# Kernel optimization log

Hardware: AMD Instinct MI355X
Metric: run time of the kernel (lower is better)

The kernel has to match this reference:

```python
import jax, jax.numpy as jnp
import numpy as np

N = 100000       # nodes
E = 3200000      # directed edges (before self-loops)
F_IN = 256       # num_node_features
HID = 8          # hidden per head (conv1)
HEADS = 8        # conv1 heads
C_OUT = 1        # conv2 out channels / heads=1


def setup_inputs() -> dict:
    key = jax.random.key(0)
    ks = jax.random.split(key, 10)
    s = 0.1
    return {
        "x": jax.random.normal(ks[0], (N, F_IN), jnp.float32),
        "edge_index": jax.random.randint(ks[1], (2, E), 0, N, dtype=jnp.int32),
        "W1": jax.random.normal(ks[2], (F_IN, HEADS * HID), jnp.float32) * s,
        "att_src1": jax.random.normal(ks[3], (HEADS, HID), jnp.float32) * s,
        "att_dst1": jax.random.normal(ks[4], (HEADS, HID), jnp.float32) * s,
        "b1": jnp.zeros((HEADS * HID,), jnp.float32),
        "W2": jax.random.normal(ks[5], (HEADS * HID, C_OUT), jnp.float32) * s,
        "att_src2": jax.random.normal(ks[6], (1, C_OUT), jnp.float32) * s,
        "att_dst2": jax.random.normal(ks[7], (1, C_OUT), jnp.float32) * s,
        "b2": jnp.zeros((C_OUT,), jnp.float32),
    }


def gat_conv(x, W, att_src, att_dst, bias, src, dst, heads, out_ch, concat):
    # PyG GATConv (eval mode): h = x @ W per head; alpha over incoming edges of dst.
    h = (x @ W).reshape(-1, heads, out_ch)                 # [N, H, C]
    a_s = jnp.einsum('nhc,hc->nh', h, att_src)             # source term
    a_d = jnp.einsum('nhc,hc->nh', h, att_dst)             # target term
    e = jax.nn.leaky_relu(a_s[src] + a_d[dst], 0.2)        # [Etot, H]
    # segment softmax over edges grouped by target node
    m = jax.ops.segment_max(e, dst, num_segments=N)
    ex = jnp.exp(e - m[dst])
    denom = jax.ops.segment_sum(ex, dst, num_segments=N)
    alpha = ex / (denom[dst] + 1e-16)                      # [Etot, H]
    out = jax.ops.segment_sum(h[src] * alpha[..., None], dst, num_segments=N)
    out = out.reshape(-1, heads * out_ch) if concat else out.mean(axis=1)
    return out + bias


def reference(x, edge_index, W1, att_src1, att_dst1, b1, W2, att_src2, att_dst2, b2):
    # add self-loops (GATConv default add_self_loops=True)
    loop = jnp.arange(N, dtype=edge_index.dtype)
    src = jnp.concatenate([edge_index[0], loop])
    dst = jnp.concatenate([edge_index[1], loop])
    # dropout layers are identity in eval mode
    h = gat_conv(x, W1, att_src1, att_dst1, b1, src, dst, HEADS, HID, True)
    h = jax.nn.elu(h)
    out = gat_conv(h, W2, att_src2, att_dst2, b2, src, dst, 1, C_OUT, False)
    return jax.nn.sigmoid(out)
```

## Files before the change

kernel.cpp:

```cpp
#include <hip/hip_runtime.h>
#include <math.h>

#define FIN 256
#define C1  64
#define NH  8
#define HID 8
#define MAXBUK 512
#define CAPLOG 14
#define SC_CHUNK 8192
#define EPT (SC_CHUNK / 512)
#define WT_STRIDE 264

typedef unsigned short ushort_t;
typedef unsigned int uint_t;
typedef __attribute__((ext_vector_type(8))) short short8;
typedef __attribute__((ext_vector_type(4))) float f32x4;

__device__ __forceinline__ ushort_t f2bf(float f) {
    uint_t u = __float_as_uint(f);
    u += 0x7fffu + ((u >> 16) & 1u);
    return (ushort_t)(u >> 16);
}
__device__ __forceinline__ uint_t packbf2(float lo, float hi) {
    return (uint_t)f2bf(lo) | ((uint_t)f2bf(hi) << 16);
}
__device__ __forceinline__ float bf_lo(uint_t w) { return __uint_as_float(w << 16); }
__device__ __forceinline__ float bf_hi(uint_t w) { return __uint_as_float(w & 0xffff0000u); }

__global__ void k_zero_i(int* __restrict__ p, int n) {
    int i = blockIdx.x * blockDim.x + threadIdx.x;
    if (i < n) p[i] = 0;
}

__global__ __launch_bounds__(512) void k_bscatter(const int* __restrict__ ei, int E, int N,
                                                  int NBUK, int* __restrict__ bkt_cnt,
                                                  uint_t* __restrict__ ebuf) {
    __shared__ int hist[MAXBUK];
    __shared__ int loff[MAXBUK];
    __shared__ int delta[MAXBUK];
    __shared__ int ssum[MAXBUK];
    __shared__ uint_t vals[SC_CHUNK];
    __shared__ ushort_t buks[SC_CHUNK];

    const int t = threadIdx.x;
    hist[t] = 0;
    __syncthreads();

    const int Etot = E + N;
    const int base0 = blockIdx.x * SC_CHUNK;
    const int lim = min(base0 + SC_CHUNK, Etot);
    const int cnt = lim - base0;

    uint_t myval[EPT];
    int myb[EPT];
#pragma unroll
    for (int i = 0; i < EPT; ++i) {
        int e = base0 + t + i * 512;
        if (e < lim) {
            int s, d;
            if (e < E) { s = ei[e]; d = ei[E + e]; } else { s = e - E; d = s; }
            myval[i] = ((uint_t)s << 8) | (uint_t)(d & 255);
            myb[i] = d >> 8;
            atomicAdd(&hist[myb[i]], 1);
        } else myb[i] = -1;
    }
    __syncthreads();

    int v = hist[t];
    ssum[t] = v;
    __syncthreads();
    for (int o = 1; o < 512; o <<= 1) {
        int add = (t >= o) ? ssum[t - o] : 0;
        __syncthreads();
        ssum[t] += add;
        __syncthreads();
    }
    loff[t] = ssum[t] - v;
    __syncthreads();

    if (t < NBUK) {
        int c = hist[t];
        if (c) delta[t] = (t << CAPLOG) + atomicAdd(&bkt_cnt[t], c) - loff[t];
    }
    __syncthreads();

#pragma unroll
    for (int i = 0; i < EPT; ++i) {
        if (myb[i] >= 0) {
            int pos = atomicAdd(&loff[myb[i]], 1);
            vals[pos] = myval[i];
            buks[pos] = (ushort_t)myb[i];
        }
    }
    __syncthreads();

    for (int i = t; i < cnt; i += 512)
        ebuf[delta[buks[i]] + i] = vals[i];
}

__global__ __launch_bounds__(512) void k_bucket_csr(const uint_t* __restrict__ ebuf,
                                                    const int* __restrict__ bkt_cnt, int N,
                                                    int* __restrict__ deg, int* __restrict__ off,
                                                    int* __restrict__ csr) {
    __shared__ int degw[8 * 256];
    __shared__ int scan[256];
    __shared__ int curl[256];
    int b = blockIdx.x;
    int t = threadIdx.x;
    int wv = t >> 6;
    int beg = b << CAPLOG;
    int end = beg + bkt_cnt[b];
    for (int i = t; i < 8 * 256; i += 512) degw[i] = 0;
    __syncthreads();
    for (int j = beg + t; j < end; j += 512) {
        uint_t v = ebuf[j];
        atomicAdd(&degw[(wv << 8) + (v & 255u)], 1);
    }
    __syncthreads();
    int v = 0;
    if (t < 256) {
#pragma unroll
        for (int w = 0; w < 8; ++w) v += degw[(w << 8) + t];
        scan[t] = v;
    }
    __syncthreads();
    for (int o = 1; o < 256; o <<= 1) {
        int a = (t < 256 && t >= o) ? scan[t - o] : 0;
        __syncthreads();
        if (t < 256) scan[t] += a;
        __syncthreads();
    }
    if (t < 256) {
        int gpos = beg + scan[t] - v;
        int node = (b << 8) + t;
        if (node < N) { off[node] = gpos; deg[node] = v; }
        curl[t] = gpos;
    }
    __syncthreads();
    for (int j = beg + t; j < end; j += 512) {
        uint_t p = ebuf[j];
        int pos = atomicAdd(&curl[p & 255u], 1);
        csr[pos] = (int)(p >> 8);
    }
}

__global__ __launch_bounds__(256) void k_gemm1(
    const float* __restrict__ x, const float* __restrict__ W,
    const float* __restrict__ att_s, const float* __restrict__ att_d,
    ushort_t* __restrict__ h1b, ushort_t* __restrict__ as1b, float* __restrict__ ad1, int N)
{
    __shared__ __align__(16) ushort_t Wt[C1 * WT_STRIDE];

    const int t = threadIdx.x;
    {
        int c4 = t >> 4;
        int k0 = t & 15;
#pragma unroll
        for (int i = 0; i < 16; ++i) {
            int k = k0 + 16 * i;
            float4 v = *reinterpret_cast<const float4*>(&W[k * C1 + c4 * 4]);
            Wt[(c4 * 4 + 0) * WT_STRIDE + k] = f2bf(v.x);
            Wt[(c4 * 4 + 1) * WT_STRIDE + k] = f2bf(v.y);
            Wt[(c4 * 4 + 2) * WT_STRIDE + k] = f2bf(v.z);
            Wt[(c4 * 4 + 3) * WT_STRIDE + k] = f2bf(v.w);
        }
    }
    __syncthreads();

    const int wv = t >> 6, l = t & 63;
    const int l15 = l & 15, q = l >> 4;
    const int nodeBase = blockIdx.x * 128 + wv * 32;

    const float* xr[2];
#pragma unroll
    for (int nt = 0; nt < 2; ++nt) {
        int node = nodeBase + nt * 16 + l15;
        if (node >= N) node = N - 1;
        xr[nt] = x + (size_t)node * FIN;
    }

    f32x4 acc[4][2];
#pragma unroll
    for (int ct = 0; ct < 4; ++ct)
#pragma unroll
        for (int nt = 0; nt < 2; ++nt)
            acc[ct][nt] = (f32x4){0.f, 0.f, 0.f, 0.f};

    for (int kk = 0; kk < 8; ++kk) {
        const int kof = kk * 32 + q * 8;
        short8 af[4];
#pragma unroll
        for (int ct = 0; ct < 4; ++ct)
            af[ct] = *reinterpret_cast<const short8*>(&Wt[(ct * 16 + l15) * WT_STRIDE + kof]);
#pragma unroll
        for (int nt = 0; nt < 2; ++nt) {
            const float4* xp = reinterpret_cast<const float4*>(xr[nt] + kof);
            float4 v0 = xp[0], v1 = xp[1];
            union { short8 s; uint_t u[4]; } bu;
            bu.u[0] = packbf2(v0.x, v0.y);
            bu.u[1] = packbf2(v0.z, v0.w);
            bu.u[2] = packbf2(v1.x, v1.y);
            bu.u[3] = packbf2(v1.z, v1.w);
#pragma unroll
            for (int ct = 0; ct < 4; ++ct)
                acc[ct][nt] = __builtin_amdgcn_mfma_f32_16x16x32_bf16(
                    af[ct], bu.s, acc[ct][nt], 0, 0, 0);
        }
    }

    float4 ats[4], atd4[4];
#pragma unroll
    for (int ct = 0; ct < 4; ++ct) {
        ats[ct]  = *reinterpret_cast<const float4*>(&att_s[ct * 16 + q * 4]);
        atd4[ct] = *reinterpret_cast<const float4*>(&att_d[ct * 16 + q * 4]);
    }
    const int hb = q >> 1;

#pragma unroll
    for (int nt = 0; nt < 2; ++nt) {
        int node = nodeBase + nt * 16 + l15;
        bool ok = node < N;
        float asp[8], adp[8];
#pragma unroll
        for (int h = 0; h < 8; ++h) { asp[h] = 0.f; adp[h] = 0.f; }
#pragma unroll
        for (int ct = 0; ct < 4; ++ct) {
            f32x4 a = acc[ct][nt];
            if (ok) {
                uint2 hv;
                hv.x = packbf2(a[0], a[1]);
                hv.y = packbf2(a[2], a[3]);
                *reinterpret_cast<uint2*>(&h1b[(size_t)node * C1 + ct * 16 + q * 4]) = hv;
            }
            int h = ct * 2 + hb;
            asp[h] = a[0] * ats[ct].x + a[1] * ats[ct].y + a[2] * ats[ct].z + a[3] * ats[ct].w;
            adp[h] = a[0] * atd4[ct].x + a[1] * atd4[ct].y + a[2] * atd4[ct].z + a[3] * atd4[ct].w;
        }
#pragma unroll
        for (int o = 16; o <= 32; o <<= 1) {
#pragma unroll
            for (int h = 0; h < 8; ++h) {
                asp[h] += __shfl_xor(asp[h], o, 64);
                adp[h] += __shfl_xor(adp[h], o, 64);
            }
        }
        if (q == 0 && ok) {
            uint4 aw;
            aw.x = packbf2(asp[0], asp[1]);
            aw.y = packbf2(asp[2], asp[3]);
            aw.z = packbf2(asp[4], asp[5]);
            aw.w = packbf2(asp[6], asp[7]);
            *reinterpret_cast<uint4*>(&as1b[(size_t)node * NH]) = aw;
            *reinterpret_cast<float4*>(&ad1[(size_t)node * NH]) =
                make_float4(adp[0], adp[1], adp[2], adp[3]);
            *reinterpret_cast<float4*>(&ad1[(size_t)node * NH + 4]) =
                make_float4(adp[4], adp[5], adp[6], adp[7]);
        }
    }
}

__global__ __launch_bounds__(256) void k_agg1(
    const int* __restrict__ csr, const int* __restrict__ off, const int* __restrict__ deg,
    const ushort_t* __restrict__ as1b, const float* __restrict__ ad1,
    const ushort_t* __restrict__ h1b,
    const float* __restrict__ b1, const float* __restrict__ W2,
    float* __restrict__ h2, int N)
{
    int idx = blockIdx.x * 256 + threadIdx.x;
    int n = idx >> 4;
    if (n >= N) return;
    int sub  = threadIdx.x & 15;
    int hp   = sub & 3;
    int slot = sub >> 2;

    int beg = off[n];
    int end = beg + deg[n];

    float adv0 = ad1[(size_t)n * NH + 2 * hp];
    float adv1 = ad1[(size_t)n * NH + 2 * hp + 1];
    float den0 = 0.f, den1 = 0.f;
    float acc[16];
#pragma unroll
    for (int k = 0; k < 16; ++k) acc[k] = 0.f;

    for (int base = beg; base < end; base += 4) {
        int j = base + slot;
        int jj = j < end ? j : end - 1;
        int s = csr[jj];
        uint_t a2 = *reinterpret_cast<const uint_t*>(&as1b[(size_t)s * NH + 2 * hp]);
        float t0 = bf_lo(a2) + adv0;
        float t1 = bf_hi(a2) + adv1;
        t0 = fmaxf(t0, 0.2f * t0);
        t1 = fmaxf(t1, 0.2f * t1);
        bool live = j < end;
        float ex0 = live ? __expf(t0) : 0.f;
        float ex1 = live ? __expf(t1) : 0.f;
        den0 += ex0; den1 += ex1;
        const uint4* hbp = reinterpret_cast<const uint4*>(&h1b[(size_t)s * C1 + hp * 16]);
        uint4 u0 = hbp[0], u1 = hbp[1];
        acc[0]  = fmaf(ex0, bf_lo(u0.x), acc[0]);
        acc[1]  = fmaf(ex0, bf_hi(u0.x), acc[1]);
        acc[2]  = fmaf(ex0, bf_lo(u0.y), acc[2]);
        acc[3]  = fmaf(ex0, bf_hi(u0.y), acc[3]);
        acc[4]  = fmaf(ex0, bf_lo(u0.z), acc[4]);
        acc[5]  = fmaf(ex0, bf_hi(u0.z), acc[5]);
        acc[6]  = fmaf(ex0, bf_lo(u0.w), acc[6]);
        acc[7]  = fmaf(ex0, bf_hi(u0.w), acc[7]);
        acc[8]  = fmaf(ex1, bf_lo(u1.x), acc[8]);
        acc[9]  = fmaf(ex1, bf_hi(u1.x), acc[9]);
        acc[10] = fmaf(ex1, bf_lo(u1.y), acc[10]);
        acc[11] = fmaf(ex1, bf_hi(u1.y), acc[11]);
        acc[12] = fmaf(ex1, bf_lo(u1.z), acc[12]);
        acc[13] = fmaf(ex1, bf_hi(u1.z), acc[13]);
        acc[14] = fmaf(ex1, bf_lo(u1.w), acc[14]);
        acc[15] = fmaf(ex1, bf_hi(u1.w), acc[15]);
    }

#pragma unroll
    for (int o = 4; o <= 8; o <<= 1) {
        den0 += __shfl_xor(den0, o, 64);
        den1 += __shfl_xor(den1, o, 64);
#pragma unroll
        for (int k = 0; k < 16; ++k) acc[k] += __shfl_xor(acc[k], o, 64);
    }

    float inv0 = 1.f / (den0 + 1e-16f);
    float inv1 = 1.f / (den1 + 1e-16f);
    const float4* bp = reinterpret_cast<const float4*>(&b1[hp * 16]);
    const float4* wp = reinterpret_cast<const float4*>(&W2[hp * 16]);
    float bb[16], ww[16];
#pragma unroll
    for (int i = 0; i < 4; ++i) {
        float4 b4 = bp[i], w4 = wp[i];
        bb[4 * i] = b4.x; bb[4 * i + 1] = b4.y; bb[4 * i + 2] = b4.z; bb[4 * i + 3] = b4.w;
        ww[4 * i] = w4.x; ww[4 * i + 1] = w4.y; ww[4 * i + 2] = w4.z; ww[4 * i + 3] = w4.w;
    }
    float p = 0.f;
#pragma unroll
    for (int k = 0; k < 16; ++k) {
        float inv = (k < 8) ? inv0 : inv1;
        float v = acc[k] * inv + bb[k];
        v = v > 0.f ? v : (__expf(v) - 1.f);
        p = fmaf(v, ww[k], p);
    }
#pragma unroll
    for (int o = 1; o <= 2; o <<= 1) p += __shfl_xor(p, o, 64);
    if (sub == 0) h2[n] = p;
}

__global__ __launch_bounds__(256) void k_agg2(
    const int* __restrict__ csr, const int* __restrict__ off, const int* __restrict__ deg,
    const float* __restrict__ h2,
    const float* __restrict__ ats2, const float* __restrict__ atd2,
    const float* __restrict__ b2, float* __restrict__ out, int N)
{
    int idx = blockIdx.x * 256 + threadIdx.x;
    int n = idx >> 4;
    int l16 = threadIdx.x & 15;
    if (n >= N) return;
    int beg = off[n];
    int end = beg + deg[n];
    float a_s = ats2[0], a_d = atd2[0];
    float adv = h2[n] * a_d;
    float den = 0.f, num = 0.f;
    for (int j = beg + l16; j < end; j += 16) {
        float hs = h2[csr[j]];
        float t = fmaf(hs, a_s, adv);
        t = fmaxf(t, 0.2f * t);
        float ex = __expf(t);
        den += ex;
        num = fmaf(ex, hs, num);
    }
#pragma unroll
    for (int o = 1; o <= 8; o <<= 1) {
        den += __shfl_xor(den, o, 64);
        num += __shfl_xor(num, o, 64);
    }
    if (l16 == 0) {
        float t = num / (den + 1e-16f) + b2[0];
        out[n] = 1.f / (1.f + __expf(-t));
    }
}

extern "C" void kernel_launch(void* const* d_in, const int* in_sizes, int n_in,
                              void* d_out, int out_size, void* d_ws, size_t ws_size,
                              hipStream_t stream)
{
    const float* x    = (const float*)d_in[0];
    const int*   ei   = (const int*)d_in[1];
    const float* W1   = (const float*)d_in[2];
    const float* ats1 = (const float*)d_in[3];
    const float* atd1 = (const float*)d_in[4];
    const float* b1   = (const float*)d_in[5];
    const float* W2   = (const float*)d_in[6];
    const float* ats2 = (const float*)d_in[7];
    const float* atd2 = (const float*)d_in[8];
    const float* b2   = (const float*)d_in[9];
    float* out = (float*)d_out;

    const int N = out_size;
    const int E = in_sizes[1] / 2;
    const int Etot = E + N;
    const int NBUK = (N + 255) >> 8;
    const size_t capElems = (size_t)NBUK << CAPLOG;

    char* base = (char*)d_ws;
    uint_t* ebuf = (uint_t*)base;
    ushort_t* h1b  = (ushort_t*)base;
    ushort_t* as1b = h1b + (size_t)N * C1;
    float* ad1 = (float*)(as1b + (size_t)N * NH);
    float* h2  = ad1 + (size_t)N * NH;
    size_t featBytes = (size_t)N * (C1 * 2 + NH * 2 + NH * 4 + 4);
    size_t unionBytes = capElems * sizeof(uint_t);
    if (featBytes > unionBytes) unionBytes = featBytes;
    unionBytes = (unionBytes + 255) & ~(size_t)255;
    int* deg     = (int*)(base + unionBytes);
    int* off     = deg + N;
    int* bkt_cnt = off + N;
    int* csr     = bkt_cnt + MAXBUK;

    k_zero_i<<<2, 256, 0, stream>>>(bkt_cnt, MAXBUK);
    k_bscatter<<<(Etot + SC_CHUNK - 1) / SC_CHUNK, 512, 0, stream>>>(ei, E, N, NBUK, bkt_cnt, ebuf);
    k_bucket_csr<<<NBUK, 512, 0, stream>>>(ebuf, bkt_cnt, N, deg, off, csr);

    k_gemm1<<<(N + 127) / 128, 256, 0, stream>>>(x, W1, ats1, atd1, h1b, as1b, ad1, N);
    k_agg1<<<(N * 16 + 255) / 256, 256, 0, stream>>>(csr, off, deg, as1b, ad1, h1b, b1, W2, h2, N);
    k_agg2<<<(N * 16 + 255) / 256, 256, 0, stream>>>(csr, off, deg, h2, ats2, atd2, b2, out, N);
}
```

Before: 335.6 us.

## Split layer-1 aggregation into four head-pair passes over planar feature layout

The GEMM now writes h1, a_src and a_dst in head-pair-major planar layout, so each head pair's features form a contiguous slab. The aggregation runs as four launches, one per head pair, with 16 lanes striding over edges and accumulating the partial layer-2 projection into h2. The aim is a smaller per-pass gather working set (a 3.2 MB slab plus attention terms) that fits in cache, trading this for four reads of the CSR and a read-modify-write of h2. It also adds an odd `bf_hi*0.f` term in one FMA.

Result: slower. 413.5 us (+23.2%).

```diff
diff --git a/kernel.cpp b/kernel.cpp
--- a/kernel.cpp
+++ b/kernel.cpp
@@ -147,7 +147,7 @@
 __global__ __launch_bounds__(256) void k_gemm1(
     const float* __restrict__ x, const float* __restrict__ W,
     const float* __restrict__ att_s, const float* __restrict__ att_d,
-    ushort_t* __restrict__ h1b, ushort_t* __restrict__ as1b, float* __restrict__ ad1, int N)
+    ushort_t* __restrict__ h1t, uint_t* __restrict__ as1t, float2* __restrict__ ad1t, int N)
 {
     __shared__ __align__(16) ushort_t Wt[C1 * WT_STRIDE];
 
@@ -230,7 +230,7 @@
                 uint2 hv;
                 hv.x = packbf2(a[0], a[1]);
                 hv.y = packbf2(a[2], a[3]);
-                *reinterpret_cast<uint2*>(&h1b[(size_t)node * C1 + ct * 16 + q * 4]) = hv;
+                *reinterpret_cast<uint2*>(&h1t[((size_t)ct * N + node) * 16 + q * 4]) = hv;
             }
             int h = ct * 2 + hb;
             asp[h] = a[0] * ats[ct].x + a[1] * ats[ct].y + a[2] * ats[ct].z + a[3] * ats[ct].w;
@@ -245,58 +245,47 @@
             }
         }
         if (q == 0 && ok) {
-            uint4 aw;
-            aw.x = packbf2(asp[0], asp[1]);
-            aw.y = packbf2(asp[2], asp[3]);
-            aw.z = packbf2(asp[4], asp[5]);
-            aw.w = packbf2(asp[6], asp[7]);
-            *reinterpret_cast<uint4*>(&as1b[(size_t)node * NH]) = aw;
-            *reinterpret_cast<float4*>(&ad1[(size_t)node * NH]) =
-                make_float4(adp[0], adp[1], adp[2], adp[3]);
-            *reinterpret_cast<float4*>(&ad1[(size_t)node * NH + 4]) =
-                make_float4(adp[4], adp[5], adp[6], adp[7]);
-        }
-    }
-}
-
-__global__ __launch_bounds__(256) void k_agg1(
+#pragma unroll
+            for (int hh = 0; hh < 4; ++hh) {
+                as1t[(size_t)hh * N + node] = packbf2(asp[2 * hh], asp[2 * hh + 1]);
+                ad1t[(size_t)hh * N + node] = make_float2(adp[2 * hh], adp[2 * hh + 1]);
+            }
+        }
+    }
+}
+
+__global__ __launch_bounds__(256) void k_agg1p(
     const int* __restrict__ csr, const int* __restrict__ off, const int* __restrict__ deg,
-    const ushort_t* __restrict__ as1b, const float* __restrict__ ad1,
-    const ushort_t* __restrict__ h1b,
-    const float* __restrict__ b1, const float* __restrict__ W2,
-    float* __restrict__ h2, int N)
+    const uint_t* __restrict__ as1s, const float2* __restrict__ ad1s,
+    const ushort_t* __restrict__ h1s,
+    const float* __restrict__ b1s, const float* __restrict__ W2s,
+    float* __restrict__ h2, int N, int first)
 {
     int idx = blockIdx.x * 256 + threadIdx.x;
     int n = idx >> 4;
     if (n >= N) return;
-    int sub  = threadIdx.x & 15;
-    int hp   = sub & 3;
-    int slot = sub >> 2;
+    int sub = threadIdx.x & 15;
 
     int beg = off[n];
     int end = beg + deg[n];
 
-    float adv0 = ad1[(size_t)n * NH + 2 * hp];
-    float adv1 = ad1[(size_t)n * NH + 2 * hp + 1];
+    float2 adv = ad1s[n];
     float den0 = 0.f, den1 = 0.f;
     float acc[16];
 #pragma unroll
     for (int k = 0; k < 16; ++k) acc[k] = 0.f;
 
-    for (int base = beg; base < end; base += 4) {
-        int j = base + slot;
-        int jj = j < end ? j : end - 1;
-        int s = csr[jj];
-        uint_t a2 = *reinterpret_cast<const uint_t*>(&as1b[(size_t)s * NH + 2 * hp]);
-        float t0 = bf_lo(a2) + adv0;
-        float t1 = bf_hi(a2) + adv1;
+    for (int j = beg + sub; j < end; j += 16) {
+        int s = csr[j];
+        uint_t a2 = as1s[s];
+        float t0 = bf_lo(a2) + adv.x;
+        float t1 = bf_hi(a2) + adv.y;
         t0 = fmaxf(t0, 0.2f * t0);
         t1 = fmaxf(t1, 0.2f * t1);
-        bool live = j < end;
-        float ex0 = live ? __expf(t0) : 0.f;
-        float ex1 = live ? __expf(t1) : 0.f;
+        float ex0 = __expf(t0);
+        float ex1 = __expf(t1);
         den0 += ex0; den1 += ex1;
-        const uint4* hbp = reinterpret_cast<const uint4*>(&h1b[(size_t)s * C1 + hp * 16]);
+        const uint4* hbp = reinterpret_cast<const uint4*>(h1s + (size_t)s * 16);
         uint4 u0 = hbp[0], u1 = hbp[1];
         acc[0]  = fmaf(ex0, bf_lo(u0.x), acc[0]);
         acc[1]  = fmaf(ex0, bf_hi(u0.x), acc[1]);
@@ -312,40 +301,31 @@
         acc[11] = fmaf(ex1, bf_hi(u1.y), acc[11]);
         acc[12] = fmaf(ex1, bf_lo(u1.z), acc[12]);
         acc[13] = fmaf(ex1, bf_hi(u1.z), acc[13]);
-        acc[14] = fmaf(ex1, bf_lo(u1.w), acc[14]);
+        acc[14] = fmaf(ex1, bf_hi(u1.w) * 0.f + bf_lo(u1.w), acc[14]);
         acc[15] = fmaf(ex1, bf_hi(u1.w), acc[15]);
     }
 
 #pragma unroll
-    for (int o = 4; o <= 8; o <<= 1) {
+    for (int o = 1; o <= 8; o <<= 1) {
         den0 += __shfl_xor(den0, o, 64);
         den1 += __shfl_xor(den1, o, 64);
 #pragma unroll
         for (int k = 0; k < 16; ++k) acc[k] += __shfl_xor(acc[k], o, 64);
     }
 
-    float inv0 = 1.f / (den0 + 1e-16f);
-    float inv1 = 1.f / (den1 + 1e-16f);
-    const float4* bp = reinterpret_cast<const float4*>(&b1[hp * 16]);
-    const float4* wp = reinterpret_cast<const float4*>(&W2[hp * 16]);
-    float bb[16], ww[16];
-#pragma unroll
-    for (int i = 0; i < 4; ++i) {
-        float4 b4 = bp[i], w4 = wp[i];
-        bb[4 * i] = b4.x; bb[4 * i + 1] = b4.y; bb[4 * i + 2] = b4.z; bb[4 * i + 3] = b4.w;
-        ww[4 * i] = w4.x; ww[4 * i + 1] = w4.y; ww[4 * i + 2] = w4.z; ww[4 * i + 3] = w4.w;
-    }
-    float p = 0.f;
-#pragma unroll
-    for (int k = 0; k < 16; ++k) {
-        float inv = (k < 8) ? inv0 : inv1;
-        float v = acc[k] * inv + bb[k];
-        v = v > 0.f ? v : (__expf(v) - 1.f);
-        p = fmaf(v, ww[k], p);
-    }
-#pragma unroll
-    for (int o = 1; o <= 2; o <<= 1) p += __shfl_xor(p, o, 64);
-    if (sub == 0) h2[n] = p;
+    if (sub == 0) {
+        float inv0 = 1.f / (den0 + 1e-16f);
+        float inv1 = 1.f / (den1 + 1e-16f);
+        float p = 0.f;
+#pragma unroll
+        for (int k = 0; k < 16; ++k) {
+            float inv = (k < 8) ? inv0 : inv1;
+            float v = acc[k] * inv + b1s[k];
+            v = v > 0.f ? v : (__expf(v) - 1.f);
+            p = fmaf(v, W2s[k], p);
+        }
+        h2[n] = (first ? 0.f : h2[n]) + p;
+    }
 }
 
 __global__ __launch_bounds__(256) void k_agg2(
@@ -406,11 +386,11 @@
 
     char* base = (char*)d_ws;
     uint_t* ebuf = (uint_t*)base;
-    ushort_t* h1b  = (ushort_t*)base;
-    ushort_t* as1b = h1b + (size_t)N * C1;
-    float* ad1 = (float*)(as1b + (size_t)N * NH);
-    float* h2  = ad1 + (size_t)N * NH;
-    size_t featBytes = (size_t)N * (C1 * 2 + NH * 2 + NH * 4 + 4);
+    ushort_t* h1t  = (ushort_t*)base;
+    uint_t* as1t   = (uint_t*)(h1t + (size_t)N * C1);
+    float2* ad1t   = (float2*)(as1t + (size_t)N * 4);
+    float* h2      = (float*)(ad1t + (size_t)N * 4);
+    size_t featBytes = (size_t)N * (C1 * 2 + 4 * 4 + 4 * 8 + 4);
     size_t unionBytes = capElems * sizeof(uint_t);
     if (featBytes > unionBytes) unionBytes = featBytes;
     unionBytes = (unionBytes + 255) & ~(size_t)255;
@@ -423,7 +403,15 @@
     k_bscatter<<<(Etot + SC_CHUNK - 1) / SC_CHUNK, 512, 0, stream>>>(ei, E, N, NBUK, bkt_cnt, ebuf);
     k_bucket_csr<<<NBUK, 512, 0, stream>>>(ebuf, bkt_cnt, N, deg, off, csr);
 
-    k_gemm1<<<(N + 127) / 128, 256, 0, stream>>>(x, W1, ats1, atd1, h1b, as1b, ad1, N);
-    k_agg1<<<(N * 16 + 255) / 256, 256, 0, stream>>>(csr, off, deg, as1b, ad1, h1b, b1, W2, h2, N);
+    k_gemm1<<<(N + 127) / 128, 256, 0, stream>>>(x, W1, ats1, atd1, h1t, as1t, ad1t, N);
+    for (int hp = 0; hp < 4; ++hp) {
+        k_agg1p<<<(N * 16 + 255) / 256, 256, 0, stream>>>(
+            csr, off, deg,
+            as1t + (size_t)hp * N,
+            ad1t + (size_t)hp * N,
+            h1t + (size_t)hp * N * 16,
+            b1 + hp * 16, W2 + hp * 16,
+            h2, N, hp == 0 ? 1 : 0);
+    }
     k_agg2<<<(N * 16 + 255) / 256, 256, 0, stream>>>(csr, off, deg, h2, ats2, atd2, b2, out, N);
 }
```

## Precompute bf16 transposed W1 globally and shrink gemm1 tiles to one node-tile per wave

Applied to the files above, without the earlier changes.

The W1 transpose and bf16 conversion moves out of every gemm1 block into a one-time prep kernel, which also zeroes the bucket counters in place of the separate zero kernel. gemm1 no longer stages W in shared memory and reads its A fragments directly from global memory, relying on L1/L2 caching. Each wave now handles 16 nodes instead of 32, so the grid doubles and per-thread accumulator registers halve. The aim is to remove per-block staging overhead and LDS use and to raise occupancy on this memory-bound GEMM. The cost is repeated global or L2 reads of W fragments and half as much reuse of each W fragment per x load.

Result: no change. 331.2 us (-1.3%).

```diff
diff --git a/kernel.cpp b/kernel.cpp
--- a/kernel.cpp
+++ b/kernel.cpp
@@ -9,7 +9,6 @@
 #define CAPLOG 14
 #define SC_CHUNK 8192
 #define EPT (SC_CHUNK / 512)
-#define WT_STRIDE 264
 
 typedef unsigned short ushort_t;
 typedef unsigned int uint_t;
@@ -27,9 +26,13 @@
 __device__ __forceinline__ float bf_lo(uint_t w) { return __uint_as_float(w << 16); }
 __device__ __forceinline__ float bf_hi(uint_t w) { return __uint_as_float(w & 0xffff0000u); }
 
-__global__ void k_zero_i(int* __restrict__ p, int n) {
-    int i = blockIdx.x * blockDim.x + threadIdx.x;
-    if (i < n) p[i] = 0;
+__global__ void k_prep(const float* __restrict__ W, ushort_t* __restrict__ Wtg,
+                       int* __restrict__ bkt_cnt) {
+    int tid = blockIdx.x * 256 + threadIdx.x;
+    if (tid < MAXBUK) bkt_cnt[tid] = 0;
+    int c = tid >> 8;
+    int k = tid & 255;
+    Wtg[c * 256 + k] = f2bf(W[k * C1 + c]);
 }
 
 __global__ __launch_bounds__(512) void k_bscatter(const int* __restrict__ ei, int E, int N,
@@ -145,67 +148,37 @@
 }
 
 __global__ __launch_bounds__(256) void k_gemm1(
-    const float* __restrict__ x, const float* __restrict__ W,
+    const float* __restrict__ x, const ushort_t* __restrict__ Wtg,
     const float* __restrict__ att_s, const float* __restrict__ att_d,
     ushort_t* __restrict__ h1b, ushort_t* __restrict__ as1b, float* __restrict__ ad1, int N)
 {
-    __shared__ __align__(16) ushort_t Wt[C1 * WT_STRIDE];
-
     const int t = threadIdx.x;
-    {
-        int c4 = t >> 4;
-        int k0 = t & 15;
-#pragma unroll
-        for (int i = 0; i < 16; ++i) {
-            int k = k0 + 16 * i;
-            float4 v = *reinterpret_cast<const float4*>(&W[k * C1 + c4 * 4]);
-            Wt[(c4 * 4 + 0) * WT_STRIDE + k] = f2bf(v.x);
-            Wt[(c4 * 4 + 1) * WT_STRIDE + k] = f2bf(v.y);
-            Wt[(c4 * 4 + 2) * WT_STRIDE + k] = f2bf(v.z);
-            Wt[(c4 * 4 + 3) * WT_STRIDE + k] = f2bf(v.w);
-        }
-    }
-    __syncthreads();
-
     const int wv = t >> 6, l = t & 63;
     const int l15 = l & 15, q = l >> 4;
-    const int nodeBase = blockIdx.x * 128 + wv * 32;
-
-    const float* xr[2];
-#pragma unroll
-    for (int nt = 0; nt < 2; ++nt) {
-        int node = nodeBase + nt * 16 + l15;
-        if (node >= N) node = N - 1;
-        xr[nt] = x + (size_t)node * FIN;
-    }
-
-    f32x4 acc[4][2];
-#pragma unroll
-    for (int ct = 0; ct < 4; ++ct)
-#pragma unroll
-        for (int nt = 0; nt < 2; ++nt)
-            acc[ct][nt] = (f32x4){0.f, 0.f, 0.f, 0.f};
+    const int node = blockIdx.x * 64 + wv * 16 + l15;
+    const bool ok = node < N;
+    const float* xr = x + (size_t)(ok ? node : N - 1) * FIN;
+
+    f32x4 acc[4];
+#pragma unroll
+    for (int ct = 0; ct < 4; ++ct) acc[ct] = (f32x4){0.f, 0.f, 0.f, 0.f};
 
     for (int kk = 0; kk < 8; ++kk) {
         const int kof = kk * 32 + q * 8;
         short8 af[4];
 #pragma unroll
         for (int ct = 0; ct < 4; ++ct)
-            af[ct] = *reinterpret_cast<const short8*>(&Wt[(ct * 16 + l15) * WT_STRIDE + kof]);
-#pragma unroll
-        for (int nt = 0; nt < 2; ++nt) {
-            const float4* xp = reinterpret_cast<const float4*>(xr[nt] + kof);
-            float4 v0 = xp[0], v1 = xp[1];
-            union { short8 s; uint_t u[4]; } bu;
-            bu.u[0] = packbf2(v0.x, v0.y);
-            bu.u[1] = packbf2(v0.z, v0.w);
-            bu.u[2] = packbf2(v1.x, v1.y);
-            bu.u[3] = packbf2(v1.z, v1.w);
-#pragma unroll
-            for (int ct = 0; ct < 4; ++ct)
-                acc[ct][nt] = __builtin_amdgcn_mfma_f32_16x16x32_bf16(
-                    af[ct], bu.s, acc[ct][nt], 0, 0, 0);
-        }
+            af[ct] = *reinterpret_cast<const short8*>(&Wtg[(ct * 16 + l15) * 256 + kof]);
+        const float4* xp = reinterpret_cast<const float4*>(xr + kof);
+        float4 v0 = xp[0], v1 = xp[1];
+        union { short8 s; uint_t u[4]; } bu;
+        bu.u[0] = packbf2(v0.x, v0.y);
+        bu.u[1] = packbf2(v0.z, v0.w);
+        bu.u[2] = packbf2(v1.x, v1.y);
+        bu.u[3] = packbf2(v1.z, v1.w);
+#pragma unroll
+        for (int ct = 0; ct < 4; ++ct)
+            acc[ct] = __builtin_amdgcn_mfma_f32_16x16x32_bf16(af[ct], bu.s, acc[ct], 0, 0, 0);
     }
 
     float4 ats[4], atd4[4];
@@ -216,46 +189,41 @@
     }
     const int hb = q >> 1;
 
-#pragma unroll
-    for (int nt = 0; nt < 2; ++nt) {
-        int node = nodeBase + nt * 16 + l15;
-        bool ok = node < N;
-        float asp[8], adp[8];
-#pragma unroll
-        for (int h = 0; h < 8; ++h) { asp[h] = 0.f; adp[h] = 0.f; }
-#pragma unroll
-        for (int ct = 0; ct < 4; ++ct) {
-            f32x4 a = acc[ct][nt];
-            if (ok) {
-                uint2 hv;
-                hv.x = packbf2(a[0], a[1]);
-                hv.y = packbf2(a[2], a[3]);
-                *reinterpret_cast<uint2*>(&h1b[(size_t)node * C1 + ct * 16 + q * 4]) = hv;
-            }
-            int h = ct * 2 + hb;
-            asp[h] = a[0] * ats[ct].x + a[1] * ats[ct].y + a[2] * ats[ct].z + a[3] * ats[ct].w;
-            adp[h] = a[0] * atd4[ct].x + a[1] * atd4[ct].y + a[2] * atd4[ct].z + a[3] * atd4[ct].w;
+    float asp[8], adp[8];
+#pragma unroll
+    for (int h = 0; h < 8; ++h) { asp[h] = 0.f; adp[h] = 0.f; }
+#pragma unroll
+    for (int ct = 0; ct < 4; ++ct) {
+        f32x4 a = acc[ct];
+        if (ok) {
+            uint2 hv;
+            hv.x = packbf2(a[0], a[1]);
+            hv.y = packbf2(a[2], a[3]);
+            *reinterpret_cast<uint2*>(&h1b[(size_t)node * C1 + ct * 16 + q * 4]) = hv;
         }
-#pragma unroll
-        for (int o = 16; o <= 32; o <<= 1) {
-#pragma unroll
-            for (int h = 0; h < 8; ++h) {
-                asp[h] += __shfl_xor(asp[h], o, 64);
-                adp[h] += __shfl_xor(adp[h], o, 64);
-            }
+        int h = ct * 2 + hb;
+        asp[h] = a[0] * ats[ct].x + a[1] * ats[ct].y + a[2] * ats[ct].z + a[3] * ats[ct].w;
+        adp[h] = a[0] * atd4[ct].x + a[1] * atd4[ct].y + a[2] * atd4[ct].z + a[3] * atd4[ct].w;
+    }
+#pragma unroll
+    for (int o = 16; o <= 32; o <<= 1) {
+#pragma unroll
+        for (int h = 0; h < 8; ++h) {
+            asp[h] += __shfl_xor(asp[h], o, 64);
+            adp[h] += __shfl_xor(adp[h], o, 64);
         }
-        if (q == 0 && ok) {
-            uint4 aw;
-            aw.x = packbf2(asp[0], asp[1]);
-            aw.y = packbf2(asp[2], asp[3]);
-            aw.z = packbf2(asp[4], asp[5]);
-            aw.w = packbf2(asp[6], asp[7]);
-            *reinterpret_cast<uint4*>(&as1b[(size_t)node * NH]) = aw;
-            *reinterpret_cast<float4*>(&ad1[(size_t)node * NH]) =
-                make_float4(adp[0], adp[1], adp[2], adp[3]);
-            *reinterpret_cast<float4*>(&ad1[(size_t)node * NH + 4]) =
-                make_float4(adp[4], adp[5], adp[6], adp[7]);
-        }
+    }
+    if (q == 0 && ok) {
+        uint4 aw;
+        aw.x = packbf2(asp[0], asp[1]);
+        aw.y = packbf2(asp[2], asp[3]);
+        aw.z = packbf2(asp[4], asp[5]);
+        aw.w = packbf2(asp[6], asp[7]);
+        *reinterpret_cast<uint4*>(&as1b[(size_t)node * NH]) = aw;
+        *reinterpret_cast<float4*>(&ad1[(size_t)node * NH]) =
+            make_float4(adp[0], adp[1], adp[2], adp[3]);
+        *reinterpret_cast<float4*>(&ad1[(size_t)node * NH + 4]) =
+            make_float4(adp[4], adp[5], adp[6], adp[7]);
     }
 }
 
@@ -418,12 +386,13 @@
     int* off     = deg + N;
     int* bkt_cnt = off + N;
     int* csr     = bkt_cnt + MAXBUK;
-
-    k_zero_i<<<2, 256, 0, stream>>>(bkt_cnt, MAXBUK);
+    ushort_t* wtg = (ushort_t*)(csr + capElems);
+
+    k_prep<<<64, 256, 0, stream>>>(W1, wtg, bkt_cnt);
     k_bscatter<<<(Etot + SC_CHUNK - 1) / SC_CHUNK, 512, 0, stream>>>(ei, E, N, NBUK, bkt_cnt, ebuf);
     k_bucket_csr<<<NBUK, 512, 0, stream>>>(ebuf, bkt_cnt, N, deg, off, csr);
 
-    k_gemm1<<<(N + 127) / 128, 256, 0, stream>>>(x, W1, ats1, atd1, h1b, as1b, ad1, N);
+    k_gemm1<<<(N + 63) / 64, 256, 0, stream>>>(x, wtg, ats1, atd1, h1b, as1b, ad1, N);
     k_agg1<<<(N * 16 + 255) / 256, 256, 0, stream>>>(csr, off, deg, as1b, ad1, h1b, b1, W2, h2, N);
     k_agg2<<<(N * 16 + 255) / 256, 256, 0, stream>>>(csr, off, deg, h2, ats2, atd2, b2, out, N);
 }
```
